# Kernel optimization log

Measured on AMD Instinct MI355X. Metric: run time of the kernel, lower is better.

## Reference

```python
import jax, jax.numpy as jnp
import numpy as np

# Multi-scale deformable attention (MSDeformableAttention from RTDETRTransformerv2)
SPATIAL = ((80, 80), (40, 40), (20, 20))  # (h, w) per level, strides 8/16/32 on 640x640
N_HEADS, N_LEVELS, N_POINTS = 8, 3, 4
D_MODEL = 256
HEAD_DIM = D_MODEL // N_HEADS


def setup_inputs() -> dict:
    key = jax.random.key(0)
    ks = jax.random.split(key, 10)
    B, Q = 16, 300
    Lv = sum(h * w for h, w in SPATIAL)  # 8400
    s = 0.02
    return {
        "query": jax.random.normal(ks[0], (B, Q, D_MODEL), jnp.float32),
        "reference_points": jax.random.uniform(ks[1], (B, Q, 4), jnp.float32),
        "value": jax.random.normal(ks[2], (B, Lv, D_MODEL), jnp.float32),
        "Wv": jax.random.normal(ks[3], (D_MODEL, D_MODEL), jnp.float32) * s,
        "bv": jnp.zeros((D_MODEL,), jnp.float32),
        "Woff": jax.random.normal(ks[4], (D_MODEL, N_HEADS * N_LEVELS * N_POINTS * 2), jnp.float32) * s,
        "boff": jax.random.normal(ks[5], (N_HEADS * N_LEVELS * N_POINTS * 2,), jnp.float32) * 0.1,
        "Wattn": jax.random.normal(ks[6], (D_MODEL, N_HEADS * N_LEVELS * N_POINTS), jnp.float32) * s,
        "battn": jnp.zeros((N_HEADS * N_LEVELS * N_POINTS,), jnp.float32),
        "Wout": jax.random.normal(ks[7], (D_MODEL, D_MODEL), jnp.float32) * s,
        "bout": jnp.zeros((D_MODEL,), jnp.float32),
    }


def _grid_sample_level(v_lvl, gx, gy, h, w):
    """Bilinear grid_sample, align_corners=False, zeros padding.

    v_lvl : (B, nH, h*w, hd) flattened per-level value map
    gx,gy : (B, nH, P) sample coords in [-1, 1]
    returns (B, nH, P, hd)
    """
    px = ((gx + 1.0) * w - 1.0) * 0.5  # pixel x
    py = ((gy + 1.0) * h - 1.0) * 0.5  # pixel y
    x0 = jnp.floor(px)
    y0 = jnp.floor(py)
    fx = px - x0
    fy = py - y0
    x0i = x0.astype(jnp.int32)
    y0i = y0.astype(jnp.int32)

    def corner(xi, yi, wgt):
        valid = (xi >= 0) & (xi < w) & (yi >= 0) & (yi < h)
        idx = jnp.clip(yi, 0, h - 1) * w + jnp.clip(xi, 0, w - 1)
        g = jnp.take_along_axis(v_lvl, idx[..., None], axis=2)  # (B,nH,P,hd)
        return g * (wgt * valid.astype(wgt.dtype))[..., None]

    return (corner(x0i, y0i, (1 - fx) * (1 - fy))
            + corner(x0i + 1, y0i, fx * (1 - fy))
            + corner(x0i, y0i + 1, (1 - fx) * fy)
            + corner(x0i + 1, y0i + 1, fx * fy))


def reference(query, reference_points, value, Wv, bv, Woff, boff, Wattn, battn, Wout, bout):
    B, Q, _ = query.shape
    # value projection -> per-head values
    v = (value @ Wv + bv).reshape(B, -1, N_HEADS, HEAD_DIM)
    # sampling offsets and attention weights from queries
    off = (query @ Woff + boff).reshape(B, Q, N_HEADS, N_LEVELS, N_POINTS, 2)
    aw = jax.nn.softmax(
        (query @ Wattn + battn).reshape(B, Q, N_HEADS, N_LEVELS * N_POINTS), axis=-1
    ).reshape(B, Q, N_HEADS, N_LEVELS, N_POINTS)
    # reference points (cx, cy) broadcast over heads/levels/points
    ref = reference_points[:, :, None, None, None, :2]
    pts = jnp.clip(ref + off, 0.0, 1.0)      # (B,Q,nH,nL,nP,2) in [0,1]
    g = pts * 2.0 - 1.0                      # grid_sample coords in [-1,1]

    out = jnp.zeros((B, Q, N_HEADS, HEAD_DIM), query.dtype)
    start = 0
    for lvl, (h, w) in enumerate(SPATIAL):
        v_lvl = v[:, start:start + h * w].transpose(0, 2, 1, 3)  # (B,nH,hw,hd)
        gl = g[:, :, :, lvl]                                     # (B,Q,nH,nP,2)
        gx = gl[..., 0].transpose(0, 2, 1, 3).reshape(B, N_HEADS, Q * N_POINTS)
        gy = gl[..., 1].transpose(0, 2, 1, 3).reshape(B, N_HEADS, Q * N_POINTS)
        sampled = _grid_sample_level(v_lvl, gx, gy, h, w)        # (B,nH,Q*nP,hd)
        sampled = sampled.reshape(B, N_HEADS, Q, N_POINTS, HEAD_DIM)
        wl = aw[:, :, :, lvl].transpose(0, 2, 1, 3)              # (B,nH,Q,nP)
        out = out + jnp.einsum('bhqpd,bhqp->bqhd', sampled, wl)
        start += h * w

    return out.reshape(B, Q, D_MODEL) @ Wout + bout
```

## Files before the change

### kernel.cpp

```cpp
#include <hip/hip_runtime.h>
#include <hip/hip_bf16.h>
#include <cstddef>

#define NB 16
#define NQ 300
#define DM 256
#define LV_ 8400

typedef __attribute__((ext_vector_type(8))) short short8;
typedef __attribute__((ext_vector_type(4))) float f32x4;

static __device__ __forceinline__ unsigned short bf16_rne(float f) {
  unsigned int u = __builtin_bit_cast(unsigned int, f);
  u += 0x7FFFu + ((u >> 16) & 1u);
  return (unsigned short)(u >> 16);
}

static __device__ __forceinline__ unsigned int pack_bf2(float a, float b) {
  __hip_bfloat162 p = __float22bfloat162_rn(make_float2(a, b));
  unsigned int u;
  __builtin_memcpy(&u, &p, 4);
  return u;
}

static __device__ __forceinline__ void gload16(const void* g, void* l) {
  __builtin_amdgcn_global_load_lds(
      (const __attribute__((address_space(1))) unsigned int*)g,
      (__attribute__((address_space(3))) unsigned int*)l, 16, 0, 0);
}

__global__ __launch_bounds__(256) void prep_kernel(
    const float* __restrict__ Wv, const float* __restrict__ Wout,
    unsigned short* __restrict__ WthP, unsigned short* __restrict__ WoutT) {
  __shared__ float tle[32][33];
  const int k0 = blockIdx.x * 32, n0 = blockIdx.y * 32;
  const int xx = threadIdx.x & 31, y4 = (threadIdx.x >> 5) * 4;
  const float* src = blockIdx.z ? Wout : Wv;
  #pragma unroll
  for (int i = 0; i < 4; ++i)
    tle[y4 + i][xx] = src[(size_t)(k0 + y4 + i) * DM + n0 + xx];
  __syncthreads();
  if (blockIdx.z == 0) {
    if (threadIdx.x < 128) {
      const int nl = threadIdx.x >> 2, q8 = threadIdx.x & 3;
      const int n = n0 + nl, yy = n >> 7, col = n & 127;
      uint4 o;
      o.x = pack_bf2(tle[q8 * 8 + 0][nl], tle[q8 * 8 + 1][nl]);
      o.y = pack_bf2(tle[q8 * 8 + 2][nl], tle[q8 * 8 + 3][nl]);
      o.z = pack_bf2(tle[q8 * 8 + 4][nl], tle[q8 * 8 + 5][nl]);
      o.w = pack_bf2(tle[q8 * 8 + 6][nl], tle[q8 * 8 + 7][nl]);
      const size_t idx = ((((size_t)yy * 8 + blockIdx.x) * 4 + q8) * 128 + col) * 8;
      *(uint4*)&WthP[idx] = o;
    }
  } else {
    #pragma unroll
    for (int i = 0; i < 4; ++i)
      WoutT[(size_t)(n0 + y4 + i) * DM + k0 + xx] = bf16_rne(tle[xx][y4 + i]);
  }
}

__global__ __launch_bounds__(256, 3) void vproj_mfma(
    const float* __restrict__ A, const unsigned short* __restrict__ WthP,
    const float* __restrict__ bias, unsigned short* __restrict__ V) {
  __shared__ float Af[2][4][128][8];
  __shared__ unsigned short Bf[2][4][128][8];
  const int tid = threadIdx.x;
  const int lane = tid & 63;
  const int wave = tid >> 6;
  const int l16 = lane & 15, q4 = lane >> 4;
  const int wr = (wave >> 1) * 64, wc = (wave & 1) * 64;

  const int b = blockIdx.x;
  const int xcd = b & 7, cidx = b >> 3;
  const int w = (xcd < 4 ? xcd * 263 : 4 * 263 + (xcd - 4) * 262) + cidx;
  const int xb = w >> 1, y = w & 1;
  const size_t row0 = (size_t)xb * 128;
  const int col0 = y * 128;

  const unsigned short* bsrc = WthP + (size_t)y * 8 * 4096;

#define STAGE(bufi, kb_) do {                                                  \
    _Pragma("unroll")                                                          \
    for (int c_ = 0; c_ < 4; ++c_) {                                           \
      const int u_ = wave * 4 + c_;                                            \
      const int row_ = c_ * 32 + (lane >> 1);                                  \
      const int h_ = lane & 1;                                                 \
      const int k_ = wave * 8 + ((h_ ^ ((row_ >> 2) & 1)) << 2);               \
      gload16(A + (row0 + row_) * DM + (kb_) * 32 + k_,                        \
              (char*)&Af[bufi][0][0][0] + u_ * 1024);                          \
    }                                                                          \
    _Pragma("unroll")                                                          \
    for (int c_ = 0; c_ < 2; ++c_) {                                           \
      const int u_ = wave * 2 + c_;                                            \
      gload16(bsrc + (size_t)(kb_) * 4096 + u_ * 512 + lane * 8,               \
              (char*)&Bf[bufi][0][0][0] + u_ * 1024);                          \
    }                                                                          \
  } while (0)

  f32x4 acc[4][4];
  #pragma unroll
  for (int i = 0; i < 4; ++i)
    #pragma unroll
    for (int j = 0; j < 4; ++j) acc[i][j] = (f32x4)0.f;

  const int swf = ((l16 >> 2) & 1) << 2;

  int buf = 0;
  STAGE(0, 0);
  __syncthreads();

  for (int kb = 0; kb < 8; ++kb) {
    if (kb < 7) STAGE(buf ^ 1, kb + 1);

    short8 bfr[4];
    #pragma unroll
    for (int j = 0; j < 4; ++j)
      bfr[j] = *(const short8*)&Bf[buf][q4][wc + j * 16 + l16][0];

    #pragma unroll
    for (int i = 0; i < 4; ++i) {
      const float* rp = &Af[buf][q4][wr + i * 16 + l16][0];
      const float4 lo = *(const float4*)(rp + swf);
      const float4 hi = *(const float4*)(rp + (4 ^ swf));
      uint4 p;
      p.x = pack_bf2(lo.x, lo.y); p.y = pack_bf2(lo.z, lo.w);
      p.z = pack_bf2(hi.x, hi.y); p.w = pack_bf2(hi.z, hi.w);
      const short8 af = __builtin_bit_cast(short8, p);
      #pragma unroll
      for (int j = 0; j < 4; ++j)
        acc[i][j] = __builtin_amdgcn_mfma_f32_16x16x32_bf16(af, bfr[j], acc[i][j], 0, 0, 0);
    }
    __syncthreads();
    buf ^= 1;
  }
#undef STAGE

  #pragma unroll
  for (int i = 0; i < 4; ++i)
    #pragma unroll
    for (int j = 0; j < 4; ++j) {
      const int col = col0 + wc + j * 16 + l16;
      const float bcol = bias[col];
      #pragma unroll
      for (int r = 0; r < 4; ++r) {
        const size_t row = row0 + wr + i * 16 + q4 * 4 + r;
        V[row * DM + col] = bf16_rne(acc[i][j][r] + bcol);
      }
    }
}

__global__ __launch_bounds__(256) void gemm_qp(
    const float* __restrict__ q,
    const float* __restrict__ Woff, const float* __restrict__ boff,
    const float* __restrict__ Wattn, const float* __restrict__ battn,
    float* __restrict__ offb, float* __restrict__ logitb) {
  const int by = blockIdx.y;
  const float* W; const float* bias; float* C; int N, c0;
  if (by < 6) { W = Woff;  bias = boff;  C = offb;   N = 192; c0 = by * 32; }
  else        { W = Wattn; bias = battn; C = logitb; N = 96;  c0 = (by - 6) * 32; }
  const int m0 = blockIdx.x * 32;

  __shared__ float As[32][33];
  __shared__ float Bs[32][33];
  const int tid = threadIdx.x;
  const int ar = tid >> 3, ak = (tid & 7) * 4;
  const int kr = tid >> 3, bc = (tid & 7) * 4;
  const int tx = tid & 15, ty = tid >> 4;

  const float* apt = q + (size_t)(m0 + ar) * DM + ak;
  float4 av = *(const float4*)apt;
  float4 wv = *(const float4*)(W + (size_t)kr * N + c0 + bc);

  float acc[2][2] = {{0.f, 0.f}, {0.f, 0.f}};
  for (int kk = 0; kk < DM; kk += 32) {
    __syncthreads();
    As[ak + 0][ar] = av.x;
    As[ak + 1][ar] = av.y;
    As[ak + 2][ar] = av.z;
    As[ak + 3][ar] = av.w;
    *(float4*)&Bs[kr][bc] = wv;
    __syncthreads();
    if (kk + 32 < DM) {
      av = *(const float4*)(apt + kk + 32);
      wv = *(const float4*)(W + (size_t)(kk + 32 + kr) * N + c0 + bc);
    }
    #pragma unroll
    for (int k = 0; k < 32; ++k) {
      const float2 a2 = *(const float2*)&As[k][ty * 2];
      const float2 b2 = *(const float2*)&Bs[k][tx * 2];
      acc[0][0] = fmaf(a2.x, b2.x, acc[0][0]);
      acc[0][1] = fmaf(a2.x, b2.y, acc[0][1]);
      acc[1][0] = fmaf(a2.y, b2.x, acc[1][0]);
      acc[1][1] = fmaf(a2.y, b2.y, acc[1][1]);
    }
  }
  const float b0 = bias[c0 + tx * 2], b1 = bias[c0 + tx * 2 + 1];
  #pragma unroll
  for (int i = 0; i < 2; ++i) {
    float2 o; o.x = acc[i][0] + b0; o.y = acc[i][1] + b1;
    *(float2*)&C[(size_t)(m0 + ty * 2 + i) * N + c0 + tx * 2] = o;
  }
}

__global__ __launch_bounds__(256) void sample_kernel(
    const float* __restrict__ refp, const unsigned short* __restrict__ v,
    const float* __restrict__ off, const float* __restrict__ logits,
    unsigned short* __restrict__ mid) {
  const int x = blockIdx.x;
  const int c8 = x & 7, kb = x >> 3;
  const int b = c8 + (kb >= 150 ? 8 : 0);
  const int qp = (kb >= 150 ? kb - 150 : kb);
  const int bq0 = b * NQ + qp * 2;
  const int t = threadIdx.x;
  __shared__ float off_sh[2][192];
  __shared__ float aw_sh[2][96];
  __shared__ int   idx_sh[2][96][4];
  __shared__ float wt_sh[2][96][4];
  __shared__ float ref_sh[2][2];

  {
    const float* osrc = off + (size_t)bq0 * 192;
    float* odst = &off_sh[0][0];
    odst[t] = osrc[t];
    if (t < 128) odst[256 + t] = osrc[256 + t];
    const float* lsrc = logits + (size_t)bq0 * 96;
    if (t < 192) (&aw_sh[0][0])[t] = lsrc[t];
    if (t < 4) ref_sh[t >> 1][t & 1] = refp[(bq0 + (t >> 1)) * 4 + (t & 1)];
  }
  __syncthreads();

  if (t < 16) {
    const int q = t >> 3, h = t & 7;
    float* aw = &aw_sh[q][h * 12];
    float m = -1e30f;
    #pragma unroll
    for (int i = 0; i < 12; ++i) m = fmaxf(m, aw[i]);
    float e[12], s = 0.f;
    #pragma unroll
    for (int i = 0; i < 12; ++i) { e[i] = __expf(aw[i] - m); s += e[i]; }
    const float inv = 1.f / s;
    #pragma unroll
    for (int i = 0; i < 12; ++i) aw[i] = e[i] * inv;
  }
  __syncthreads();

  if (t < 192) {
    const int q = t / 96, r = t - q * 96;
    const int h = r / 12, lp = r - h * 12;
    const int l = lp >> 2, p = lp & 3;
    const int LH[3] = {80, 40, 20};
    const int LS[3] = {0, 6400, 8000};
    const int hh = LH[l], ww = LH[l], st = LS[l];
    const int oi = ((h * 3 + l) * 4 + p) * 2;
    const float aw = aw_sh[q][h * 12 + lp];
    const float sx = fminf(fmaxf(ref_sh[q][0] + off_sh[q][oi], 0.f), 1.f);
    const float sy = fminf(fmaxf(ref_sh[q][1] + off_sh[q][oi + 1], 0.f), 1.f);
    const float px = sx * (float)ww - 0.5f;
    const float py = sy * (float)hh - 0.5f;
    const float x0f = floorf(px), y0f = floorf(py);
    const float fx = px - x0f, fy = py - y0f;
    const int x0 = (int)x0f, y0 = (int)y0f;
    const int x1 = x0 + 1, y1 = y0 + 1;
    const bool vx0 = (x0 >= 0) & (x0 < ww), vx1 = (x1 >= 0) & (x1 < ww);
    const bool vy0 = (y0 >= 0) & (y0 < hh), vy1 = (y1 >= 0) & (y1 < hh);
    const int x0c = min(max(x0, 0), ww - 1), x1c = min(max(x1, 0), ww - 1);
    const int y0c = min(max(y0, 0), hh - 1), y1c = min(max(y1, 0), hh - 1);
    idx_sh[q][r][0] = st + y0c * ww + x0c;
    idx_sh[q][r][1] = st + y0c * ww + x1c;
    idx_sh[q][r][2] = st + y1c * ww + x0c;
    idx_sh[q][r][3] = st + y1c * ww + x1c;
    wt_sh[q][r][0] = aw * (1.f - fx) * (1.f - fy) * ((vx0 & vy0) ? 1.f : 0.f);
    wt_sh[q][r][1] = aw * fx * (1.f - fy) * ((vx1 & vy0) ? 1.f : 0.f);
    wt_sh[q][r][2] = aw * (1.f - fx) * fy * ((vx0 & vy1) ? 1.f : 0.f);
    wt_sh[q][r][3] = aw * fx * fy * ((vx1 & vy1) ? 1.f : 0.f);
  }
  __syncthreads();

  const int q = t >> 7, h = (t >> 4) & 7, dp = t & 15;
  const unsigned short* vb = v + (size_t)b * LV_ * DM + h * 32 + dp * 2;
  float ax = 0.f, ay = 0.f;
  #pragma unroll
  for (int r = 0; r < 12; ++r) {
    const int rr = h * 12 + r;
    #pragma unroll
    for (int cc = 0; cc < 4; ++cc) {
      const int id = idx_sh[q][rr][cc];
      const float w = wt_sh[q][rr][cc];
      const unsigned int u = *(const unsigned int*)(vb + (size_t)id * DM);
      ax = fmaf(w, __builtin_bit_cast(float, u << 16), ax);
      ay = fmaf(w, __builtin_bit_cast(float, u & 0xFFFF0000u), ay);
    }
  }
  unsigned short* mp = mid + (size_t)(bq0 + q) * DM + h * 32 + dp * 2;
  *(unsigned int*)mp = pack_bf2(ax, ay);
}

__global__ __launch_bounds__(256) void outp_mfma(
    const unsigned short* __restrict__ midb, const unsigned short* __restrict__ WoutT,
    const float* __restrict__ bias, float* __restrict__ out) {
  __shared__ short Ah[4][64][8];
  __shared__ short Bh[4][64][8];
  const int tid = threadIdx.x;
  const int lane = tid & 63;
  const int wave = tid >> 6;
  const int l16 = lane & 15, q4 = lane >> 4;
  const int wc = wave * 16;
  const int m0 = blockIdx.x * 64, col0 = blockIdx.y * 64;

  const int r = tid >> 2, ch = tid & 3;
  const unsigned short* apt = midb + (size_t)(m0 + r) * DM + ch * 8;
  const unsigned short* wpt = WoutT + (size_t)(col0 + r) * DM + ch * 8;
  uint4 am = *(const uint4*)apt;
  uint4 wm = *(const uint4*)wpt;

  f32x4 acc[4];
  #pragma unroll
  for (int i = 0; i < 4; ++i) acc[i] = (f32x4)0.f;

  for (int kk = 0; kk < DM; kk += 32) {
    __syncthreads();
    *(uint4*)&Ah[ch][r][0] = am;
    *(uint4*)&Bh[ch][r][0] = wm;
    __syncthreads();
    if (kk + 32 < DM) {
      am = *(const uint4*)(apt + kk + 32);
      wm = *(const uint4*)(wpt + kk + 32);
    }
    const short8 bfrag = *(const short8*)&Bh[q4][wc + l16][0];
    #pragma unroll
    for (int i = 0; i < 4; ++i) {
      const short8 af = *(const short8*)&Ah[q4][i * 16 + l16][0];
      acc[i] = __builtin_amdgcn_mfma_f32_16x16x32_bf16(af, bfrag, acc[i], 0, 0, 0);
    }
  }

  const int col = col0 + wc + l16;
  const float bcol = bias[col];
  #pragma unroll
  for (int i = 0; i < 4; ++i)
    #pragma unroll
    for (int rr = 0; rr < 4; ++rr)
      out[(size_t)(m0 + i * 16 + q4 * 4 + rr) * DM + col] = acc[i][rr] + bcol;
}

extern "C" void kernel_launch(void* const* d_in, const int* in_sizes, int n_in,
                              void* d_out, int out_size, void* d_ws, size_t ws_size,
                              hipStream_t stream) {
  (void)in_sizes; (void)n_in; (void)out_size; (void)ws_size;
  const float* query = (const float*)d_in[0];
  const float* refp  = (const float*)d_in[1];
  const float* value = (const float*)d_in[2];
  const float* Wv    = (const float*)d_in[3];
  const float* bv    = (const float*)d_in[4];
  const float* Woff  = (const float*)d_in[5];
  const float* boff  = (const float*)d_in[6];
  const float* Wattn = (const float*)d_in[7];
  const float* battn = (const float*)d_in[8];
  const float* Wout  = (const float*)d_in[9];
  const float* bout  = (const float*)d_in[10];
  float* out = (float*)d_out;

  char* ws = (char*)d_ws;
  unsigned short* v_bf  = (unsigned short*)ws;
  unsigned short* WthP  = (unsigned short*)(ws + 68812800);
  unsigned short* WoutT = (unsigned short*)(ws + 68943872);
  float* offb   = (float*)(ws + 69074944);
  float* logitb = (float*)(ws + 72761344);
  unsigned short* midb = (unsigned short*)(ws + 74604544);

  prep_kernel<<<dim3(8, 8, 2), 256, 0, stream>>>(Wv, Wout, WthP, WoutT);
  gemm_qp<<<dim3(150, 9), 256, 0, stream>>>(query, Woff, boff, Wattn, battn, offb, logitb);
  vproj_mfma<<<2100, 256, 0, stream>>>(value, WthP, bv, v_bf);
  sample_kernel<<<2400, 256, 0, stream>>>(refp, v_bf, offb, logitb, midb);
  outp_mfma<<<dim3(75, 4), 256, 0, stream>>>(midb, WoutT, bout, out);
}
```

Measured before the change: 291.4 us.

## Triple-buffer A tiles in value projection GEMM with split vmcnt waits

Restructures the vproj_mfma K-loop so the fp32 A operand is prefetched two stages ahead in a triple-buffered LDS ring while B stays double-buffered. Full __syncthreads are replaced by explicit s_waitcnt vmcnt plus s_barrier, and the loop is fully unrolled. This aims to hide global-to-LDS latency behind MFMA work. In exchange it uses more LDS, so occupancy drops from 3 to 2 blocks per CU, and the correctness of the vmcnt(4) count depends on the exact number of loads in flight.

After: 301.3 us. +3.4%, slower.

```diff
diff --git a/kernel.cpp b/kernel.cpp
--- a/kernel.cpp
+++ b/kernel.cpp
@@ -59,10 +59,10 @@
   }
 }
 
-__global__ __launch_bounds__(256, 3) void vproj_mfma(
+__global__ __launch_bounds__(256, 2) void vproj_mfma(
     const float* __restrict__ A, const unsigned short* __restrict__ WthP,
     const float* __restrict__ bias, unsigned short* __restrict__ V) {
-  __shared__ float Af[2][4][128][8];
+  __shared__ float Af[3][4][128][8];
   __shared__ unsigned short Bf[2][4][128][8];
   const int tid = threadIdx.x;
   const int lane = tid & 63;
@@ -79,7 +79,7 @@
 
   const unsigned short* bsrc = WthP + (size_t)y * 8 * 4096;
 
-#define STAGE(bufi, kb_) do {                                                  \
+#define STAGE_A(bufi, kb_) do {                                                \
     _Pragma("unroll")                                                          \
     for (int c_ = 0; c_ < 4; ++c_) {                                           \
       const int u_ = wave * 4 + c_;                                            \
@@ -89,6 +89,8 @@
       gload16(A + (row0 + row_) * DM + (kb_) * 32 + k_,                        \
               (char*)&Af[bufi][0][0][0] + u_ * 1024);                          \
     }                                                                          \
+  } while (0)
+#define STAGE_B(bufi, kb_) do {                                                \
     _Pragma("unroll")                                                          \
     for (int c_ = 0; c_ < 2; ++c_) {                                           \
       const int u_ = wave * 2 + c_;                                            \
@@ -105,21 +107,30 @@
 
   const int swf = ((l16 >> 2) & 1) << 2;
 
-  int buf = 0;
-  STAGE(0, 0);
-  __syncthreads();
-
+  STAGE_A(0, 0);
+  STAGE_B(0, 0);
+  STAGE_A(1, 1);
+
+  #pragma unroll
   for (int kb = 0; kb < 8; ++kb) {
-    if (kb < 7) STAGE(buf ^ 1, kb + 1);
-
+    if (kb < 7) {
+      asm volatile("s_waitcnt vmcnt(4)" ::: "memory");
+    } else {
+      asm volatile("s_waitcnt vmcnt(0)" ::: "memory");
+    }
+    __builtin_amdgcn_s_barrier();
+    if (kb + 1 < 8) STAGE_B((kb + 1) & 1, kb + 1);
+    if (kb + 2 < 8) STAGE_A((kb + 2) % 3, kb + 2);
+
+    const int ba = kb % 3, bb = kb & 1;
     short8 bfr[4];
     #pragma unroll
     for (int j = 0; j < 4; ++j)
-      bfr[j] = *(const short8*)&Bf[buf][q4][wc + j * 16 + l16][0];
+      bfr[j] = *(const short8*)&Bf[bb][q4][wc + j * 16 + l16][0];
 
     #pragma unroll
     for (int i = 0; i < 4; ++i) {
-      const float* rp = &Af[buf][q4][wr + i * 16 + l16][0];
+      const float* rp = &Af[ba][q4][wr + i * 16 + l16][0];
       const float4 lo = *(const float4*)(rp + swf);
       const float4 hi = *(const float4*)(rp + (4 ^ swf));
       uint4 p;
@@ -130,10 +141,9 @@
       for (int j = 0; j < 4; ++j)
         acc[i][j] = __builtin_amdgcn_mfma_f32_16x16x32_bf16(af, bfr[j], acc[i][j], 0, 0, 0);
     }
-    __syncthreads();
-    buf ^= 1;
-  }
-#undef STAGE
+  }
+#undef STAGE_A
+#undef STAGE_B
 
   #pragma unroll
   for (int i = 0; i < 4; ++i)
```

## Preload full B tile in LDS and stream A directly into registers

Applied to the files above, without the earlier changes.

The value-projection GEMM now loads the whole 128-column bf16 weight slice into LDS once at kernel start, instead of double-buffering it per k-block. The fp32 A fragments are read straight from global memory into registers with a one-step register prefetch, replacing the LDS staging path. This drops the per-iteration barriers and the LDS round trip for A. In exchange it uses more LDS (64KB), lowers the launch-bounds occupancy hint from 3 to 2 blocks, and uses more registers for the prefetch buffers.

Measured after the change: 311.4 us. 1.07x slower.

```diff
diff --git a/kernel.cpp b/kernel.cpp
--- a/kernel.cpp
+++ b/kernel.cpp
@@ -59,11 +59,10 @@
   }
 }
 
-__global__ __launch_bounds__(256, 3) void vproj_mfma(
+__global__ __launch_bounds__(256, 2) void vproj_mfma(
     const float* __restrict__ A, const unsigned short* __restrict__ WthP,
     const float* __restrict__ bias, unsigned short* __restrict__ V) {
-  __shared__ float Af[2][4][128][8];
-  __shared__ unsigned short Bf[2][4][128][8];
+  __shared__ unsigned short Bh[8][4][128][8];
   const int tid = threadIdx.x;
   const int lane = tid & 63;
   const int wave = tid >> 6;
@@ -77,51 +76,52 @@
   const size_t row0 = (size_t)xb * 128;
   const int col0 = y * 128;
 
-  const unsigned short* bsrc = WthP + (size_t)y * 8 * 4096;
-
-#define STAGE(bufi, kb_) do {                                                  \
+  {
+    const unsigned short* bsrc = WthP + (size_t)y * 32768;
+    #pragma unroll
+    for (int u = 0; u < 16; ++u) {
+      const int chunk = u * 4 + wave;
+      gload16(bsrc + chunk * 512 + lane * 8,
+              (char*)&Bh[0][0][0][0] + chunk * 1024);
+    }
+  }
+
+  f32x4 acc[4][4];
+  #pragma unroll
+  for (int i = 0; i < 4; ++i)
+    #pragma unroll
+    for (int j = 0; j < 4; ++j) acc[i][j] = (f32x4)0.f;
+
+  const float* ap = A + (row0 + wr + l16) * DM + q4 * 8;
+
+#define LOADA(dst, kb_) do {                                                   \
     _Pragma("unroll")                                                          \
-    for (int c_ = 0; c_ < 4; ++c_) {                                           \
-      const int u_ = wave * 4 + c_;                                            \
-      const int row_ = c_ * 32 + (lane >> 1);                                  \
-      const int h_ = lane & 1;                                                 \
-      const int k_ = wave * 8 + ((h_ ^ ((row_ >> 2) & 1)) << 2);               \
-      gload16(A + (row0 + row_) * DM + (kb_) * 32 + k_,                        \
-              (char*)&Af[bufi][0][0][0] + u_ * 1024);                          \
-    }                                                                          \
-    _Pragma("unroll")                                                          \
-    for (int c_ = 0; c_ < 2; ++c_) {                                           \
-      const int u_ = wave * 2 + c_;                                            \
-      gload16(bsrc + (size_t)(kb_) * 4096 + u_ * 512 + lane * 8,               \
-              (char*)&Bf[bufi][0][0][0] + u_ * 1024);                          \
+    for (int i_ = 0; i_ < 4; ++i_) {                                           \
+      const float* p_ = ap + (size_t)(i_ * 16) * DM + (kb_) * 32;              \
+      dst[i_ * 2 + 0] = *(const float4*)p_;                                    \
+      dst[i_ * 2 + 1] = *(const float4*)(p_ + 4);                              \
     }                                                                          \
   } while (0)
 
-  f32x4 acc[4][4];
-  #pragma unroll
-  for (int i = 0; i < 4; ++i)
-    #pragma unroll
-    for (int j = 0; j < 4; ++j) acc[i][j] = (f32x4)0.f;
-
-  const int swf = ((l16 >> 2) & 1) << 2;
-
-  int buf = 0;
-  STAGE(0, 0);
-  __syncthreads();
-
+  float4 la[8];
+  LOADA(la, 0);
+
+  __syncthreads();
+
+  #pragma unroll 1
   for (int kb = 0; kb < 8; ++kb) {
-    if (kb < 7) STAGE(buf ^ 1, kb + 1);
+    float4 ln[8];
+    if (kb < 7) LOADA(ln, kb + 1);
 
     short8 bfr[4];
     #pragma unroll
     for (int j = 0; j < 4; ++j)
-      bfr[j] = *(const short8*)&Bf[buf][q4][wc + j * 16 + l16][0];
+      bfr[j] = *(const short8*)&Bh[kb][q4][wc + j * 16 + l16][0];
 
     #pragma unroll
     for (int i = 0; i < 4; ++i) {
-      const float* rp = &Af[buf][q4][wr + i * 16 + l16][0];
-      const float4 lo = *(const float4*)(rp + swf);
-      const float4 hi = *(const float4*)(rp + (4 ^ swf));
+      const float4 lo = la[i * 2 + 0];
+      const float4 hi = la[i * 2 + 1];
       uint4 p;
       p.x = pack_bf2(lo.x, lo.y); p.y = pack_bf2(lo.z, lo.w);
       p.z = pack_bf2(hi.x, hi.y); p.w = pack_bf2(hi.z, hi.w);
@@ -130,10 +130,13 @@
       for (int j = 0; j < 4; ++j)
         acc[i][j] = __builtin_amdgcn_mfma_f32_16x16x32_bf16(af, bfr[j], acc[i][j], 0, 0, 0);
     }
-    __syncthreads();
-    buf ^= 1;
-  }
-#undef STAGE
+
+    if (kb < 7) {
+      #pragma unroll
+      for (int u = 0; u < 8; ++u) la[u] = ln[u];
+    }
+  }
+#undef LOADA
 
   #pragma unroll
   for (int i = 0; i < 4; ++i)
```
